# Kernel tuning notes

Measured on AMD Instinct MI355X. Metric: run time of the kernel, lower is better.

## Reference

```python
import jax, jax.numpy as jnp
import numpy as np

DIM = 1024
HEADS = 16
DIM_HEAD = 64
INNER = HEADS * DIM_HEAD
EPS_NORM = 1e-12  # F.normalize eps
LN_EPS = 1e-5     # torch F.layer_norm default eps


def setup_inputs() -> dict:
    key = jax.random.key(0)
    ks = jax.random.split(key, 6)
    x = jax.random.normal(ks[0], (8, 1024, DIM), dtype=jnp.float32)
    ln_gamma = jnp.ones((DIM,), jnp.float32)
    q_gamma = jnp.ones((HEADS, 1, DIM_HEAD), jnp.float32)
    k_gamma = jnp.ones((HEADS, 1, DIM_HEAD), jnp.float32)
    # nn.Linear default init ~ U(-1/sqrt(fan_in), 1/sqrt(fan_in))
    w_qkv = jax.random.uniform(ks[1], (DIM, 3 * INNER), jnp.float32, -1.0, 1.0) / np.sqrt(DIM)
    w_out = jax.random.uniform(ks[2], (INNER, DIM), jnp.float32, -1.0, 1.0) / np.sqrt(INNER)
    return {"x": x, "ln_gamma": ln_gamma, "q_gamma": q_gamma, "k_gamma": k_gamma,
            "w_qkv": w_qkv, "w_out": w_out}


def _layer_norm(x, gamma):
    mu = jnp.mean(x, axis=-1, keepdims=True)
    var = jnp.var(x, axis=-1, keepdims=True)
    return (x - mu) * jax.lax.rsqrt(var + LN_EPS) * gamma  # beta is zeros buffer


def _rms(x, gamma):
    # F.normalize(x, dim=-1) * sqrt(d) * gamma
    n = jnp.linalg.norm(x, axis=-1, keepdims=True)
    normed = x / jnp.maximum(n, EPS_NORM)
    return normed * (DIM_HEAD ** 0.5) * gamma


def reference(x, ln_gamma, q_gamma, k_gamma, w_qkv, w_out):
    b, n, _ = x.shape
    h, d = HEADS, DIM_HEAD
    xn = _layer_norm(x, ln_gamma)
    qkv = xn @ w_qkv  # [b, n, 3*inner]
    q, k, v = jnp.split(qkv, 3, axis=-1)
    # b n (h d) -> b h n d
    to_heads = lambda t: t.reshape(b, n, h, d).transpose(0, 2, 1, 3)
    q, k, v = to_heads(q), to_heads(k), to_heads(v)
    q = _rms(q, q_gamma)
    k = _rms(k, k_gamma)
    dots = jnp.einsum('bhid,bhjd->bhij', q, k)  # no extra scale (scale baked into RMSNorm)
    attn = jax.nn.softmax(dots, axis=-1)
    out = jnp.einsum('bhij,bhjd->bhid', attn, v)
    out = out.transpose(0, 2, 1, 3).reshape(b, n, h * d)
    return out @ w_out
```

## Files before the change

kernel.cpp:

```cpp
#include <hip/hip_runtime.h>
#include <hip/hip_bf16.h>
#include <math.h>

#define DIMX   1024
#define HEADS  16
#define DH     64
#define NB     8
#define NSEQ   1024
#define ROWS   (NB * NSEQ)
#define QKVW   (3 * DIMX)
#define LOG2E  1.44269504088896f

typedef _Float16 half8 __attribute__((ext_vector_type(8)));
typedef _Float16 half4 __attribute__((ext_vector_type(4)));
typedef float floatx4 __attribute__((ext_vector_type(4)));

#define GLD_LDS16(gptr, lptr) __builtin_amdgcn_global_load_lds( \
    (const __attribute__((address_space(1))) void*)(gptr),      \
    (__attribute__((address_space(3))) void*)(lptr), 16, 0, 0)

__device__ __forceinline__ float fexp2(float x) {
#if __has_builtin(__builtin_amdgcn_exp2f)
    return __builtin_amdgcn_exp2f(x);
#else
    return __expf(x * 0.69314718056f);
#endif
}

__global__ __launch_bounds__(256) void lnw_kernel(const float* __restrict__ x,
                                                  const float* __restrict__ gamma,
                                                  const float* __restrict__ Wq,
                                                  const float* __restrict__ Wo,
                                                  _Float16* __restrict__ xn,
                                                  _Float16* __restrict__ WqT,
                                                  _Float16* __restrict__ WoT) {
    __shared__ float tile[32][33];
    __shared__ float sbuf[4], ssbuf[4];
    int t = threadIdx.x;

    if (blockIdx.x < ROWS) {
        int row = blockIdx.x;
        const float* xr = x + (size_t)row * DIMX;
        _Float16* xo = xn + (size_t)row * DIMX;

        float4 v = ((const float4*)xr)[t];
        float s  = v.x + v.y + v.z + v.w;
        float ss = v.x*v.x + v.y*v.y + v.z*v.z + v.w*v.w;
        #pragma unroll
        for (int o = 32; o > 0; o >>= 1) {
            s  += __shfl_down(s, o);
            ss += __shfl_down(ss, o);
        }
        int lane = t & 63, wid = t >> 6;
        if (lane == 0) { sbuf[wid] = s; ssbuf[wid] = ss; }
        __syncthreads();
        if (t == 0) {
            float a = 0.f, b2 = 0.f;
            for (int i = 0; i < 4; i++) { a += sbuf[i]; b2 += ssbuf[i]; }
            sbuf[0] = a; ssbuf[0] = b2;
        }
        __syncthreads();
        float mean = sbuf[0] * (1.0f / DIMX);
        float var  = ssbuf[0] * (1.0f / DIMX) - mean * mean;
        float rstd = rsqrtf(var + 1e-5f);

        float4 g = ((const float4*)gamma)[t];
        half4 o;
        o.x = (_Float16)((v.x - mean) * rstd * g.x);
        o.y = (_Float16)((v.y - mean) * rstd * g.y);
        o.z = (_Float16)((v.z - mean) * rstd * g.z);
        o.w = (_Float16)((v.w - mean) * rstd * g.w);
        *(half4*)(xo + t * 4) = o;
    } else {
        int idx = blockIdx.x - ROWS;
        int bx = idx & 127, by = idx >> 7;
        const float* W; _Float16* WT; int N, n0;
        if (bx < 96) { W = Wq; WT = WqT; N = QKVW; n0 = bx * 32; }
        else         { W = Wo; WT = WoT; N = DIMX; n0 = (bx - 96) * 32; }
        int k0 = by * 32;
        int tx = t & 31, ty = t >> 5;
        #pragma unroll
        for (int i = 0; i < 32; i += 8)
            tile[ty + i][tx] = W[(size_t)(k0 + ty + i) * N + n0 + tx];
        __syncthreads();
        #pragma unroll
        for (int i = 0; i < 32; i += 8)
            WT[(size_t)(n0 + ty + i) * 1024 + k0 + tx] = (_Float16)tile[tx][ty + i];
    }
}

__global__ __launch_bounds__(256) void hgemm_qkv(const _Float16* __restrict__ A,
                                                 const _Float16* __restrict__ BT,
                                                 const float* __restrict__ qg,
                                                 const float* __restrict__ kg,
                                                 _Float16* __restrict__ qf,
                                                 _Float16* __restrict__ kf,
                                                 _Float16* __restrict__ vt) {
    __shared__ _Float16 As[128 * 64];
    __shared__ _Float16 Bs[128 * 64];
    const int K = DIMX;

    int t = threadIdx.x;
    int wave = t >> 6, lane = t & 63;
    int quad = lane >> 4, l16 = lane & 15;
    int wm = (wave >> 1) * 64;
    int wn = (wave & 1) * 64;
    size_t m0 = (size_t)blockIdx.y * 128, n0 = (size_t)blockIdx.x * 128;

    floatx4 acc[4][4] = {};

    int sr = t >> 3, sg = t & 7;
    int swz = sg ^ (sr & 7);
    const _Float16* ag = A  + (m0 + sr) * (size_t)K + swz * 8;
    const _Float16* bg = BT + (n0 + sr) * (size_t)K + swz * 8;
    char* lA = (char*)As + wave * 1024;
    char* lB = (char*)Bs + wave * 1024;

    for (int k0 = 0; k0 < K; k0 += 64) {
        #pragma unroll
        for (int i = 0; i < 4; i++) {
            GLD_LDS16(ag + (size_t)(i * 32) * K + k0, lA + i * 4096);
            GLD_LDS16(bg + (size_t)(i * 32) * K + k0, lB + i * 4096);
        }
        __syncthreads();

        half8 af[2][4], bf[2][4];
        #pragma unroll
        for (int kk = 0; kk < 2; kk++) {
            #pragma unroll
            for (int mf = 0; mf < 4; mf++)
                af[kk][mf] = *(const half8*)&As[(wm + mf * 16 + l16) * 64
                                 + (((kk * 4 + quad) ^ (l16 & 7)) * 8)];
            #pragma unroll
            for (int nf = 0; nf < 4; nf++)
                bf[kk][nf] = *(const half8*)&Bs[(wn + nf * 16 + l16) * 64
                                 + (((kk * 4 + quad) ^ (l16 & 7)) * 8)];
        }

        #pragma unroll
        for (int kk = 0; kk < 2; kk++)
            #pragma unroll
            for (int mf = 0; mf < 4; mf++)
                #pragma unroll
                for (int nf = 0; nf < 4; nf++)
                    acc[mf][nf] = __builtin_amdgcn_mfma_f32_16x16x32_f16(
                        bf[kk][nf], af[kk][mf], acc[mf][nf], 0, 0, 0);
        __syncthreads();
    }

    int which = (int)(n0 >> 10);
    int nloc  = ((int)n0 & 1023) + wn;
    int h = nloc >> 6;

    if (which < 2) {
        const float* g = (which == 0) ? qg : kg;
        float emul = (which == 0) ? LOG2E : 1.0f;
        _Float16* dstbuf = (which == 0) ? qf : kf;
        #pragma unroll
        for (int mf = 0; mf < 4; mf++) {
            size_t tok = m0 + wm + mf * 16 + l16;
            int b = (int)(tok >> 10), ntk = (int)(tok & 1023);
            _Float16* dst = dstbuf + (((size_t)(b * 16 + h)) * 1024 + ntk) * 64;
            float ss = 0.f;
            #pragma unroll
            for (int nf = 0; nf < 4; nf++)
                #pragma unroll
                for (int r = 0; r < 4; r++) ss += acc[mf][nf][r] * acc[mf][nf][r];
            ss += __shfl_xor(ss, 16);
            ss += __shfl_xor(ss, 32);
            float scale = 8.0f * emul / fmaxf(sqrtf(ss), 1e-12f);
            #pragma unroll
            for (int nf = 0; nf < 4; nf++) {
                half4 p;
                #pragma unroll
                for (int r = 0; r < 4; r++)
                    p[r] = (_Float16)(acc[mf][nf][r] * scale *
                                      g[h * 64 + nf * 16 + quad * 4 + r]);
                *(half4*)(dst + nf * 16 + quad * 4) = p;
            }
        }
    } else {
        #pragma unroll
        for (int mf = 0; mf < 4; mf++) {
            size_t tok = m0 + wm + mf * 16 + l16;
            int b = (int)(tok >> 10), ntk = (int)(tok & 1023);
            int nt = ntk >> 6;
            _Float16* vd = vt + ((size_t)((b * 16 + h) * 16 + nt) * 64) * 64
                              + mf * 16 + l16;
            #pragma unroll
            for (int nf = 0; nf < 4; nf++)
                #pragma unroll
                for (int r = 0; r < 4; r++)
                    vd[(size_t)(nf * 16 + quad * 4 + r) * 64] =
                        (_Float16)acc[mf][nf][r];
        }
    }
}

__global__ __launch_bounds__(256, 3) void flash_kernel(const _Float16* __restrict__ qf,
                                                       const _Float16* __restrict__ kf,
                                                       const _Float16* __restrict__ vt,
                                                       _Float16* __restrict__ obuf) {
    __shared__ _Float16 Ks[2][64 * 64];
    __shared__ _Float16 VTs[2][64 * 64];
    __shared__ _Float16 Ps[4][16][68];

    int t = threadIdx.x;
    int wave = t >> 6, lane = t & 63;
    int quad = lane >> 4, l16 = lane & 15;
    int bh = blockIdx.x & 127, qt = blockIdx.x >> 7;

    const _Float16* qb = qf + ((size_t)bh * 1024 + qt * 128) * 64;
    const _Float16* kb = kf + (size_t)bh * 65536;
    const _Float16* vb = vt + (size_t)bh * 65536;

    half8 aq[2][2];
    #pragma unroll
    for (int st = 0; st < 2; st++) {
        const _Float16* qrow = qb + (wave * 32 + st * 16 + l16) * 64;
        aq[st][0] = *(const half8*)(qrow + quad * 8);
        aq[st][1] = *(const half8*)(qrow + 32 + quad * 8);
    }

    floatx4 o[2][4] = {};
    float m_i[2] = {-INFINITY, -INFINITY};
    float l_i[2] = {0.f, 0.f};

    int sr = t >> 3;
    int sg = t & 7;
    int swz = sg ^ (sr & 7);

    #pragma unroll
    for (int i = 0; i < 2; i++) {
        GLD_LDS16(kb + (i * 32 + sr) * 64 + swz * 8, (char*)Ks[0]  + wave * 1024 + i * 4096);
        GLD_LDS16(vb + (i * 32 + sr) * 64 + swz * 8, (char*)VTs[0] + wave * 1024 + i * 4096);
    }

    for (int kt = 0; kt < 16; kt++) {
        int cur = kt & 1;
        __syncthreads();

        if (kt < 15) {
            const _Float16* kn = kb + (size_t)(kt + 1) * 4096;
            const _Float16* vn = vb + (size_t)(kt + 1) * 4096;
            #pragma unroll
            for (int i = 0; i < 2; i++) {
                GLD_LDS16(kn + (i * 32 + sr) * 64 + swz * 8,
                          (char*)Ks[cur ^ 1]  + wave * 1024 + i * 4096);
                GLD_LDS16(vn + (i * 32 + sr) * 64 + swz * 8,
                          (char*)VTs[cur ^ 1] + wave * 1024 + i * 4096);
            }
        }

        #pragma unroll
        for (int st = 0; st < 2; st++) {
            floatx4 sc[4] = {};
            #pragma unroll
            for (int kc = 0; kc < 2; kc++) {
                #pragma unroll
                for (int nf = 0; nf < 4; nf++) {
                    half8 ak = *(const half8*)&Ks[cur][(nf * 16 + l16) * 64
                                    + (((kc * 4 + quad) ^ (l16 & 7)) * 8)];
                    sc[nf] = __builtin_amdgcn_mfma_f32_16x16x32_f16(
                        ak, aq[st][kc], sc[nf], 0, 0, 0);
                }
            }

            float mx = sc[0][0];
            #pragma unroll
            for (int nf = 0; nf < 4; nf++)
                #pragma unroll
                for (int r = 0; r < 4; r++) mx = fmaxf(mx, sc[nf][r]);
            mx = fmaxf(mx, __shfl_xor(mx, 16));
            mx = fmaxf(mx, __shfl_xor(mx, 32));
            if (mx > m_i[st]) {
                float alpha = fexp2(m_i[st] - mx);
                l_i[st] *= alpha;
                #pragma unroll
                for (int nf = 0; nf < 4; nf++) o[st][nf] *= alpha;
                m_i[st] = mx;
            }
            float mcur = m_i[st];
            float psum = 0.f;
            #pragma unroll
            for (int nf = 0; nf < 4; nf++)
                #pragma unroll
                for (int r = 0; r < 4; r++) {
                    float p = fexp2(sc[nf][r] - mcur);
                    sc[nf][r] = p;
                    psum += p;
                }
            l_i[st] += psum;

            #pragma unroll
            for (int nf = 0; nf < 4; nf++) {
                half4 p4;
                #pragma unroll
                for (int r = 0; r < 4; r++) p4[r] = (_Float16)sc[nf][r];
                *(half4*)&Ps[wave][l16][nf * 16 + quad * 4] = p4;
            }

            #pragma unroll
            for (int kc = 0; kc < 2; kc++) {
                half4 p0 = *(const half4*)&Ps[wave][l16][kc * 32 + quad * 8];
                half4 p1 = *(const half4*)&Ps[wave][l16][kc * 32 + quad * 8 + 4];
                half8 bp;
                #pragma unroll
                for (int j = 0; j < 4; j++) { bp[j] = p0[j]; bp[4 + j] = p1[j]; }
                #pragma unroll
                for (int nf = 0; nf < 4; nf++) {
                    half8 av = *(const half8*)&VTs[cur][(nf * 16 + l16) * 64
                                    + (((kc * 4 + quad) ^ (l16 & 7)) * 8)];
                    o[st][nf] = __builtin_amdgcn_mfma_f32_16x16x32_f16(
                        av, bp, o[st][nf], 0, 0, 0);
                }
            }
        }
    }

    int b = bh >> 4, h = bh & 15;
    #pragma unroll
    for (int st = 0; st < 2; st++) {
        float lsum = l_i[st];
        lsum += __shfl_xor(lsum, 16);
        lsum += __shfl_xor(lsum, 32);
        float inv = 1.0f / lsum;
        size_t row = (size_t)b * NSEQ + qt * 128 + wave * 32 + st * 16 + l16;
        #pragma unroll
        for (int nf = 0; nf < 4; nf++) {
            half4 o4;
            #pragma unroll
            for (int r = 0; r < 4; r++) o4[r] = (_Float16)(o[st][nf][r] * inv);
            *(half4*)(obuf + row * 1024 + h * 64 + nf * 16 + quad * 4) = o4;
        }
    }
}

__global__ __launch_bounds__(256) void hgemm_out(const _Float16* __restrict__ A,
                                                 const _Float16* __restrict__ BT,
                                                 float* __restrict__ C) {
    __shared__ _Float16 As[128 * 64];
    __shared__ _Float16 Bs[128 * 64];
    const int K = DIMX, N = DIMX;

    int t = threadIdx.x;
    int wave = t >> 6, lane = t & 63;
    int quad = lane >> 4, l16 = lane & 15;
    int wm = (wave >> 1) * 64, wn = (wave & 1) * 64;
    size_t m0 = (size_t)blockIdx.y * 128, n0 = (size_t)blockIdx.x * 128;

    floatx4 acc[4][4] = {};

    int sr = t >> 3, sg = t & 7;
    int swz = sg ^ (sr & 7);
    const _Float16* ag = A  + (m0 + sr) * (size_t)K + swz * 8;
    const _Float16* bg = BT + (n0 + sr) * (size_t)K + swz * 8;
    char* lA = (char*)As + wave * 1024;
    char* lB = (char*)Bs + wave * 1024;

    for (int k0 = 0; k0 < K; k0 += 64) {
        #pragma unroll
        for (int i = 0; i < 4; i++) {
            GLD_LDS16(ag + (size_t)(i * 32) * K + k0, lA + i * 4096);
            GLD_LDS16(bg + (size_t)(i * 32) * K + k0, lB + i * 4096);
        }
        __syncthreads();

        half8 af[2][4], bf[2][4];
        #pragma unroll
        for (int kk = 0; kk < 2; kk++) {
            #pragma unroll
            for (int mf = 0; mf < 4; mf++)
                af[kk][mf] = *(const half8*)&As[(wm + mf * 16 + l16) * 64
                                 + (((kk * 4 + quad) ^ (l16 & 7)) * 8)];
            #pragma unroll
            for (int nf = 0; nf < 4; nf++)
                bf[kk][nf] = *(const half8*)&Bs[(wn + nf * 16 + l16) * 64
                                 + (((kk * 4 + quad) ^ (l16 & 7)) * 8)];
        }

        #pragma unroll
        for (int kk = 0; kk < 2; kk++)
            #pragma unroll
            for (int mf = 0; mf < 4; mf++)
                #pragma unroll
                for (int nf = 0; nf < 4; nf++)
                    acc[mf][nf] = __builtin_amdgcn_mfma_f32_16x16x32_f16(
                        bf[kk][nf], af[kk][mf], acc[mf][nf], 0, 0, 0);
        __syncthreads();
    }

    #pragma unroll
    for (int mf = 0; mf < 4; mf++) {
        size_t tok = m0 + wm + mf * 16 + l16;
        #pragma unroll
        for (int nf = 0; nf < 4; nf++)
            *(floatx4*)(C + tok * N + n0 + wn + nf * 16 + quad * 4) = acc[mf][nf];
    }
}

extern "C" void kernel_launch(void* const* d_in, const int* in_sizes, int n_in,
                              void* d_out, int out_size, void* d_ws, size_t ws_size,
                              hipStream_t stream) {
    const float* x     = (const float*)d_in[0];
    const float* ln_g  = (const float*)d_in[1];
    const float* q_g   = (const float*)d_in[2];
    const float* k_g   = (const float*)d_in[3];
    const float* w_qkv = (const float*)d_in[4];
    const float* w_out = (const float*)d_in[5];
    float* out = (float*)d_out;

    char* base = (char*)d_ws;
    _Float16* xn    = (_Float16*)(base);
    _Float16* wqkvT = (_Float16*)(base + (16ull << 20));
    _Float16* woutT = (_Float16*)(base + (22ull << 20));
    _Float16* qf    = (_Float16*)(base + (24ull << 20));
    _Float16* kf    = (_Float16*)(base + (40ull << 20));
    _Float16* vt    = (_Float16*)(base + (56ull << 20));
    _Float16* obuf  = (_Float16*)(base + (72ull << 20));

    lnw_kernel<<<ROWS + 4096, 256, 0, stream>>>(x, ln_g, w_qkv, w_out,
                                                xn, wqkvT, woutT);

    dim3 g1(QKVW / 128, ROWS / 128);
    hgemm_qkv<<<g1, 256, 0, stream>>>(xn, wqkvT, q_g, k_g, qf, kf, vt);

    flash_kernel<<<NB * HEADS * (NSEQ / 128), 256, 0, stream>>>(qf, kf, vt, obuf);

    dim3 g2(DIMX / 128, ROWS / 128);
    hgemm_out<<<g2, 256, 0, stream>>>(obuf, woutT, out);
}
```

Baseline: 250.0 us.

## Double-buffer GEMM LDS tiles, use wave-per-row layernorm, stage V transpose via LDS

Both fp16 GEMMs now use two LDS buffers, so the next K-tile's async global-to-LDS load is issued before the current tile's MFMAs and one barrier per iteration is dropped. This is meant to overlap memory latency with compute, at the cost of doubling LDS per block, which may lower occupancy. Layernorm now gives each row to a single wave with an xor-shuffle reduction, removing block barriers and shared-memory reductions. The V-transpose store in the QKV epilogue is staged through padded LDS so global writes become coalesced 16-byte stores.

```diff
diff --git a/kernel.cpp b/kernel.cpp
--- a/kernel.cpp
+++ b/kernel.cpp
@@ -35,44 +35,43 @@
                                                   _Float16* __restrict__ WqT,
                                                   _Float16* __restrict__ WoT) {
     __shared__ float tile[32][33];
-    __shared__ float sbuf[4], ssbuf[4];
     int t = threadIdx.x;
 
-    if (blockIdx.x < ROWS) {
-        int row = blockIdx.x;
+    if (blockIdx.x < ROWS / 4) {
+        int wave = t >> 6, lane = t & 63;
+        int row = blockIdx.x * 4 + wave;
         const float* xr = x + (size_t)row * DIMX;
         _Float16* xo = xn + (size_t)row * DIMX;
 
-        float4 v = ((const float4*)xr)[t];
-        float s  = v.x + v.y + v.z + v.w;
-        float ss = v.x*v.x + v.y*v.y + v.z*v.z + v.w*v.w;
+        float4 v[4];
+        float s = 0.f, ss = 0.f;
+        #pragma unroll
+        for (int i = 0; i < 4; i++) {
+            v[i] = ((const float4*)xr)[lane + 64 * i];
+            s  += v[i].x + v[i].y + v[i].z + v[i].w;
+            ss += v[i].x*v[i].x + v[i].y*v[i].y + v[i].z*v[i].z + v[i].w*v[i].w;
+        }
         #pragma unroll
         for (int o = 32; o > 0; o >>= 1) {
-            s  += __shfl_down(s, o);
-            ss += __shfl_down(ss, o);
-        }
-        int lane = t & 63, wid = t >> 6;
-        if (lane == 0) { sbuf[wid] = s; ssbuf[wid] = ss; }
-        __syncthreads();
-        if (t == 0) {
-            float a = 0.f, b2 = 0.f;
-            for (int i = 0; i < 4; i++) { a += sbuf[i]; b2 += ssbuf[i]; }
-            sbuf[0] = a; ssbuf[0] = b2;
-        }
-        __syncthreads();
-        float mean = sbuf[0] * (1.0f / DIMX);
-        float var  = ssbuf[0] * (1.0f / DIMX) - mean * mean;
+            s  += __shfl_xor(s, o);
+            ss += __shfl_xor(ss, o);
+        }
+        float mean = s * (1.0f / DIMX);
+        float var  = ss * (1.0f / DIMX) - mean * mean;
         float rstd = rsqrtf(var + 1e-5f);
 
-        float4 g = ((const float4*)gamma)[t];
-        half4 o;
-        o.x = (_Float16)((v.x - mean) * rstd * g.x);
-        o.y = (_Float16)((v.y - mean) * rstd * g.y);
-        o.z = (_Float16)((v.z - mean) * rstd * g.z);
-        o.w = (_Float16)((v.w - mean) * rstd * g.w);
-        *(half4*)(xo + t * 4) = o;
+        #pragma unroll
+        for (int i = 0; i < 4; i++) {
+            float4 g = ((const float4*)gamma)[lane + 64 * i];
+            half4 o;
+            o.x = (_Float16)((v[i].x - mean) * rstd * g.x);
+            o.y = (_Float16)((v[i].y - mean) * rstd * g.y);
+            o.z = (_Float16)((v[i].z - mean) * rstd * g.z);
+            o.w = (_Float16)((v[i].w - mean) * rstd * g.w);
+            *(half4*)(xo + (lane + 64 * i) * 4) = o;
+        }
     } else {
-        int idx = blockIdx.x - ROWS;
+        int idx = blockIdx.x - ROWS / 4;
         int bx = idx & 127, by = idx >> 7;
         const float* W; _Float16* WT; int N, n0;
         if (bx < 96) { W = Wq; WT = WqT; N = QKVW; n0 = bx * 32; }
@@ -96,8 +95,8 @@
                                                  _Float16* __restrict__ qf,
                                                  _Float16* __restrict__ kf,
                                                  _Float16* __restrict__ vt) {
-    __shared__ _Float16 As[128 * 64];
-    __shared__ _Float16 Bs[128 * 64];
+    __shared__ _Float16 As[2][128 * 64];
+    __shared__ _Float16 Bs[2][128 * 64];
     const int K = DIMX;
 
     int t = threadIdx.x;
@@ -113,27 +112,38 @@
     int swz = sg ^ (sr & 7);
     const _Float16* ag = A  + (m0 + sr) * (size_t)K + swz * 8;
     const _Float16* bg = BT + (n0 + sr) * (size_t)K + swz * 8;
-    char* lA = (char*)As + wave * 1024;
-    char* lB = (char*)Bs + wave * 1024;
-
-    for (int k0 = 0; k0 < K; k0 += 64) {
-        #pragma unroll
-        for (int i = 0; i < 4; i++) {
-            GLD_LDS16(ag + (size_t)(i * 32) * K + k0, lA + i * 4096);
-            GLD_LDS16(bg + (size_t)(i * 32) * K + k0, lB + i * 4096);
-        }
+
+    #pragma unroll
+    for (int i = 0; i < 4; i++) {
+        GLD_LDS16(ag + (size_t)(i * 32) * K, (char*)As[0] + wave * 1024 + i * 4096);
+        GLD_LDS16(bg + (size_t)(i * 32) * K, (char*)Bs[0] + wave * 1024 + i * 4096);
+    }
+
+    for (int kt = 0; kt < 16; kt++) {
+        int cur = kt & 1;
         __syncthreads();
 
+        if (kt < 15) {
+            int k0 = (kt + 1) * 64;
+            #pragma unroll
+            for (int i = 0; i < 4; i++) {
+                GLD_LDS16(ag + (size_t)(i * 32) * K + k0,
+                          (char*)As[cur ^ 1] + wave * 1024 + i * 4096);
+                GLD_LDS16(bg + (size_t)(i * 32) * K + k0,
+                          (char*)Bs[cur ^ 1] + wave * 1024 + i * 4096);
+            }
+        }
+
         half8 af[2][4], bf[2][4];
         #pragma unroll
         for (int kk = 0; kk < 2; kk++) {
             #pragma unroll
             for (int mf = 0; mf < 4; mf++)
-                af[kk][mf] = *(const half8*)&As[(wm + mf * 16 + l16) * 64
+                af[kk][mf] = *(const half8*)&As[cur][(wm + mf * 16 + l16) * 64
                                  + (((kk * 4 + quad) ^ (l16 & 7)) * 8)];
             #pragma unroll
             for (int nf = 0; nf < 4; nf++)
-                bf[kk][nf] = *(const half8*)&Bs[(wn + nf * 16 + l16) * 64
+                bf[kk][nf] = *(const half8*)&Bs[cur][(wn + nf * 16 + l16) * 64
                                  + (((kk * 4 + quad) ^ (l16 & 7)) * 8)];
         }
 
@@ -145,7 +155,6 @@
                 for (int nf = 0; nf < 4; nf++)
                     acc[mf][nf] = __builtin_amdgcn_mfma_f32_16x16x32_f16(
                         bf[kk][nf], af[kk][mf], acc[mf][nf], 0, 0, 0);
-        __syncthreads();
     }
 
     int which = (int)(n0 >> 10);
@@ -180,19 +189,27 @@
             }
         }
     } else {
-        #pragma unroll
-        for (int mf = 0; mf < 4; mf++) {
-            size_t tok = m0 + wm + mf * 16 + l16;
-            int b = (int)(tok >> 10), ntk = (int)(tok & 1023);
-            int nt = ntk >> 6;
-            _Float16* vd = vt + ((size_t)((b * 16 + h) * 16 + nt) * 64) * 64
-                              + mf * 16 + l16;
+        __syncthreads();
+        _Float16* myT = ((wave < 2) ? (_Float16*)As : (_Float16*)Bs)
+                        + (wave & 1) * (64 * 68);
+        #pragma unroll
+        for (int mf = 0; mf < 4; mf++)
             #pragma unroll
             for (int nf = 0; nf < 4; nf++)
                 #pragma unroll
                 for (int r = 0; r < 4; r++)
-                    vd[(size_t)(nf * 16 + quad * 4 + r) * 64] =
+                    myT[(nf * 16 + quad * 4 + r) * 68 + mf * 16 + l16] =
                         (_Float16)acc[mf][nf][r];
+        size_t tok0 = m0 + wm;
+        int b = (int)(tok0 >> 10), ntk0 = (int)(tok0 & 1023);
+        int nt = ntk0 >> 6;
+        _Float16* vbase = vt + ((size_t)((b * 16 + h) * 16 + nt) * 64) * 64;
+        int rr = lane >> 3, gg = lane & 7;
+        #pragma unroll
+        for (int j = 0; j < 8; j++) {
+            int d2 = j * 8 + rr;
+            half8 v8 = *(const half8*)&myT[d2 * 68 + gg * 8];
+            *(half8*)(vbase + d2 * 64 + gg * 8) = v8;
         }
     }
 }
@@ -339,8 +356,8 @@
 __global__ __launch_bounds__(256) void hgemm_out(const _Float16* __restrict__ A,
                                                  const _Float16* __restrict__ BT,
                                                  float* __restrict__ C) {
-    __shared__ _Float16 As[128 * 64];
-    __shared__ _Float16 Bs[128 * 64];
+    __shared__ _Float16 As[2][128 * 64];
+    __shared__ _Float16 Bs[2][128 * 64];
     const int K = DIMX, N = DIMX;
 
     int t = threadIdx.x;
@@ -355,27 +372,38 @@
     int swz = sg ^ (sr & 7);
     const _Float16* ag = A  + (m0 + sr) * (size_t)K + swz * 8;
     const _Float16* bg = BT + (n0 + sr) * (size_t)K + swz * 8;
-    char* lA = (char*)As + wave * 1024;
-    char* lB = (char*)Bs + wave * 1024;
-
-    for (int k0 = 0; k0 < K; k0 += 64) {
-        #pragma unroll
-        for (int i = 0; i < 4; i++) {
-            GLD_LDS16(ag + (size_t)(i * 32) * K + k0, lA + i * 4096);
-            GLD_LDS16(bg + (size_t)(i * 32) * K + k0, lB + i * 4096);
-        }
+
+    #pragma unroll
+    for (int i = 0; i < 4; i++) {
+        GLD_LDS16(ag + (size_t)(i * 32) * K, (char*)As[0] + wave * 1024 + i * 4096);
+        GLD_LDS16(bg + (size_t)(i * 32) * K, (char*)Bs[0] + wave * 1024 + i * 4096);
+    }
+
+    for (int kt = 0; kt < 16; kt++) {
+        int cur = kt & 1;
         __syncthreads();
 
+        if (kt < 15) {
+            int k0 = (kt + 1) * 64;
+            #pragma unroll
+            for (int i = 0; i < 4; i++) {
+                GLD_LDS16(ag + (size_t)(i * 32) * K + k0,
+                          (char*)As[cur ^ 1] + wave * 1024 + i * 4096);
+                GLD_LDS16(bg + (size_t)(i * 32) * K + k0,
+                          (char*)Bs[cur ^ 1] + wave * 1024 + i * 4096);
+            }
+        }
+
         half8 af[2][4], bf[2][4];
         #pragma unroll
         for (int kk = 0; kk < 2; kk++) {
             #pragma unroll
             for (int mf = 0; mf < 4; mf++)
-                af[kk][mf] = *(const half8*)&As[(wm + mf * 16 + l16) * 64
+                af[kk][mf] = *(const half8*)&As[cur][(wm + mf * 16 + l16) * 64
                                  + (((kk * 4 + quad) ^ (l16 & 7)) * 8)];
             #pragma unroll
             for (int nf = 0; nf < 4; nf++)
-                bf[kk][nf] = *(const half8*)&Bs[(wn + nf * 16 + l16) * 64
+                bf[kk][nf] = *(const half8*)&Bs[cur][(wn + nf * 16 + l16) * 64
                                  + (((kk * 4 + quad) ^ (l16 & 7)) * 8)];
         }
 
@@ -387,7 +415,6 @@
                 for (int nf = 0; nf < 4; nf++)
                     acc[mf][nf] = __builtin_amdgcn_mfma_f32_16x16x32_f16(
                         bf[kk][nf], af[kk][mf], acc[mf][nf], 0, 0, 0);
-        __syncthreads();
     }
 
     #pragma unroll
@@ -419,8 +446,8 @@
     _Float16* vt    = (_Float16*)(base + (56ull << 20));
     _Float16* obuf  = (_Float16*)(base + (72ull << 20));
 
-    lnw_kernel<<<ROWS + 4096, 256, 0, stream>>>(x, ln_g, w_qkv, w_out,
-                                                xn, wqkvT, woutT);
+    lnw_kernel<<<ROWS / 4 + 4096, 256, 0, stream>>>(x, ln_g, w_qkv, w_out,
+                                                    xn, wqkvT, woutT);
 
     dim3 g1(QKVW / 128, ROWS / 128);
     hgemm_qkv<<<g1, 256, 0, stream>>>(xn, wqkvT, q_g, k_g, qf, kf, vt);
```

Measured after the change: 254.0 us. About the same (+1.6%).
